# Performance work log

Measured on AMD Instinct MI355X. Metric: run time of the kernel, lower is better.

Reference implementation:

```python
import jax, jax.numpy as jnp
import numpy as np

EMBED_DIM = 1024
NUM_HEADS = 16
HEAD_DIM = EMBED_DIM // NUM_HEADS
SCALE = 1.0 / np.sqrt(HEAD_DIM)


def _quant_linear(x, w, b):
    # Per-tensor symmetric int8 quantize -> dequantize -> GEMM (faithful to QuantizedLinear)
    s = jnp.max(jnp.abs(w)) / 127.0
    w_dq = jnp.clip(jnp.round(w / s), -128.0, 127.0) * s
    return jnp.einsum('bse,oe->bso', x, w_dq) + b


def setup_inputs() -> dict:
    key = jax.random.key(0)
    ks = jax.random.split(key, 7)
    B, S, E = 2, 2048, EMBED_DIM
    return {
        'query': jax.random.normal(ks[0], (B, S, E), dtype=jnp.float32),
        'key': jax.random.normal(ks[1], (B, S, E), dtype=jnp.float32),
        'value': jax.random.normal(ks[2], (B, S, E), dtype=jnp.float32),
        'Wq': jax.random.normal(ks[3], (E, E), dtype=jnp.float32) * 0.02,
        'bq': jnp.zeros((E,), dtype=jnp.float32),
        'Wk': jax.random.normal(ks[4], (E, E), dtype=jnp.float32) * 0.02,
        'bk': jnp.zeros((E,), dtype=jnp.float32),
        'Wv': jax.random.normal(ks[5], (E, E), dtype=jnp.float32) * 0.02,
        'bv': jnp.zeros((E,), dtype=jnp.float32),
        'Wo': jax.random.normal(ks[6], (E, E), dtype=jnp.float32) * 0.02,
        'bo': jnp.zeros((E,), dtype=jnp.float32),
    }


def reference(query, key, value, Wq, bq, Wk, bk, Wv, bv, Wo, bo):
    B, S, E = query.shape
    H, D = NUM_HEADS, HEAD_DIM
    Q = _quant_linear(query, Wq, bq).reshape(B, S, H, D).transpose(0, 2, 1, 3)
    K = _quant_linear(key, Wk, bk).reshape(B, S, H, D).transpose(0, 2, 1, 3)
    V = _quant_linear(value, Wv, bv).reshape(B, S, H, D).transpose(0, 2, 1, 3)
    # [B,H,S,S] unfused attention scores
    scores = jnp.einsum('bhqd,bhkd->bhqk', Q, K) * SCALE
    attn = jax.nn.softmax(scores, axis=-1)  # dropout is identity at inference
    out = jnp.einsum('bhqk,bhkd->bhqd', attn, V)
    out = out.transpose(0, 2, 1, 3).reshape(B, S, E)
    return _quant_linear(out, Wo, bo)
```

## Files before the change

kernel.cpp:

```cpp
#include <hip/hip_runtime.h>
#include <math.h>

#define S_LEN 2048
#define EMB   1024
#define NHEAD 16
#define HDIM  64
#define MTOT  4096
#define EXP2_SCALE 0.18033688011112042f

typedef __attribute__((ext_vector_type(8))) short bf16x8;
typedef __attribute__((ext_vector_type(8))) _Float16 f16x8;
typedef __attribute__((ext_vector_type(4))) float f32x4;

#if __has_builtin(__builtin_amdgcn_exp2f)
#define FEXP2(x) __builtin_amdgcn_exp2f(x)
#else
#define FEXP2(x) exp2f(x)
#endif

__device__ __forceinline__ short f2bf(float f) {
  union { float f; unsigned u; } v; v.f = f;
  unsigned r = v.u + 0x7fffu + ((v.u >> 16) & 1u);
  return (short)(r >> 16);
}
__device__ __forceinline__ float bf2f(short s) {
  union { float f; unsigned u; } v; v.u = ((unsigned)(unsigned short)s) << 16;
  return v.f;
}
__device__ __forceinline__ short f2h(float f) {
  union { _Float16 h; short s; } u; u.h = (_Float16)f; return u.s;
}
__device__ __forceinline__ unsigned pkbf(float e0, float e1) {
  unsigned a = __float_as_uint(e1) + 0x8000u;
  unsigned b = __float_as_uint(e0) + 0x8000u;
  return __builtin_amdgcn_perm(a, b, 0x07060302u);
}

__device__ __forceinline__ void gload_lds16(const void* g, void* l) {
  __builtin_amdgcn_global_load_lds(
      (const __attribute__((address_space(1))) void*)g,
      (__attribute__((address_space(3))) void*)l, 16, 0, 0);
}

__global__ void wabsmax_k(const float* __restrict__ W0, const float* __restrict__ W1,
                          const float* __restrict__ W2, const float* __restrict__ W3,
                          unsigned* __restrict__ scaleU) {
  int w = blockIdx.x & 3;
  int part = blockIdx.x >> 2;
  const float* W = (w == 0) ? W0 : (w == 1) ? W1 : (w == 2) ? W2 : W3;
  float m = 0.f;
  int base = part * 16384;
#pragma unroll
  for (int p = 0; p < 16; ++p) {
    const float4 v = *(const float4*)&W[base + p * 1024 + threadIdx.x * 4];
    m = fmaxf(m, fmaxf(fmaxf(fabsf(v.x), fabsf(v.y)), fmaxf(fabsf(v.z), fabsf(v.w))));
  }
  __shared__ float red[256];
  red[threadIdx.x] = m;
  __syncthreads();
  for (int s = 128; s > 0; s >>= 1) {
    if (threadIdx.x < s) red[threadIdx.x] = fmaxf(red[threadIdx.x], red[threadIdx.x + s]);
    __syncthreads();
  }
  if (threadIdx.x == 0) atomicMax(&scaleU[w], __float_as_uint(red[0]));
}

__global__ void wquant_k(const float* __restrict__ W0, const float* __restrict__ W1,
                         const float* __restrict__ W2, const float* __restrict__ W3,
                         short* __restrict__ Q0, short* __restrict__ Q1,
                         short* __restrict__ Q2, short* __restrict__ Q3,
                         const unsigned* __restrict__ scaleU, float* __restrict__ sVal) {
  int w = blockIdx.y;
  const float* W = (w == 0) ? W0 : (w == 1) ? W1 : (w == 2) ? W2 : W3;
  short* Q = (w == 0) ? Q0 : (w == 1) ? Q1 : (w == 2) ? Q2 : Q3;
  float s = __uint_as_float(scaleU[w]) * (1.0f / 127.0f);
  if (blockIdx.x == 0 && threadIdx.x == 0) sVal[w] = s;
  int idx = (blockIdx.x * 256 + threadIdx.x) * 4;
  float4 v = *(const float4*)&W[idx];
  float qx = fminf(fmaxf(rintf(v.x / s), -128.f), 127.f);
  float qy = fminf(fmaxf(rintf(v.y / s), -128.f), 127.f);
  float qz = fminf(fmaxf(rintf(v.z / s), -128.f), 127.f);
  float qw = fminf(fmaxf(rintf(v.w / s), -128.f), 127.f);
  short4 q;
  if (w == 3) { q.x = f2h(qx); q.y = f2h(qy); q.z = f2h(qz); q.w = f2h(qw); }
  else        { q.x = f2bf(qx); q.y = f2bf(qy); q.z = f2bf(qz); q.w = f2bf(qw); }
  *(short4*)&Q[idx] = q;
}

__global__ void acast_k(const float* __restrict__ A0, const float* __restrict__ A1,
                        const float* __restrict__ A2,
                        short* __restrict__ H0, short* __restrict__ H1,
                        short* __restrict__ H2) {
  int w = blockIdx.y;
  const float* A = (w == 0) ? A0 : (w == 1) ? A1 : A2;
  short* H = (w == 0) ? H0 : (w == 1) ? H1 : H2;
  int idx = (blockIdx.x * 256 + threadIdx.x) * 4;
  float4 v = *(const float4*)&A[idx];
  short4 h;
  h.x = f2bf(v.x); h.y = f2bf(v.y); h.z = f2bf(v.z); h.w = f2bf(v.w);
  *(short4*)&H[idx] = h;
}

__device__ __forceinline__ void gemm_core(
    const short* __restrict__ Ah, const short* __restrict__ Bq, int m0, int n0,
    short* AhS, short* BsS, f32x4 acc[4][4]) {
  const int tid = threadIdx.x;
  const int lane = tid & 63, wave = tid >> 6;
  const int quad = lane >> 4, l16 = lane & 15;
  const int wm = wave >> 1, wn = wave & 1;

  const int swrow = lane >> 2, swcol = (lane & 3) * 8;
  const short* agh = Ah + (m0 + wave * 32 + swrow) * 1024 + swcol;
  const short* bgp = Bq + (n0 + wave * 32 + swrow) * 1024 + swcol;
  short* sA0 = AhS + wave * 1024;
  short* sB0 = BsS + wave * 1024;

  for (int k0 = 0; k0 < 1024; k0 += 32) {
    __syncthreads();
    gload_lds16(agh + k0,             sA0);
    gload_lds16(agh + 16 * 1024 + k0, sA0 + 512);
    gload_lds16(bgp + k0,             sB0);
    gload_lds16(bgp + 16 * 1024 + k0, sB0 + 512);
    __syncthreads();
    bf16x8 ah[4], bb[4];
#pragma unroll
    for (int mi = 0; mi < 4; ++mi) {
      int row = wm * 64 + mi * 16 + l16;
      ah[mi] = *(const bf16x8*)&AhS[row * 32 + quad * 8];
    }
#pragma unroll
    for (int ni = 0; ni < 4; ++ni) {
      int row = wn * 64 + ni * 16 + l16;
      bb[ni] = *(const bf16x8*)&BsS[row * 32 + quad * 8];
    }
#pragma unroll
    for (int mi = 0; mi < 4; ++mi)
#pragma unroll
      for (int ni = 0; ni < 4; ++ni)
        acc[mi][ni] = __builtin_amdgcn_mfma_f32_16x16x32_bf16(ah[mi], bb[ni], acc[mi][ni], 0, 0, 0);
  }
}

__global__ __launch_bounds__(256, 3) void gemm_qkv(
    const short* __restrict__ QA, const short* __restrict__ KA, const short* __restrict__ VA,
    const short* __restrict__ WqQ, const short* __restrict__ WkQ, const short* __restrict__ WvQ,
    const float* __restrict__ sVal,
    const float* __restrict__ bq, const float* __restrict__ bk, const float* __restrict__ bv,
    short* __restrict__ Qh, short* __restrict__ Kh, short* __restrict__ Vh) {
  __shared__ __align__(16) short AhS[128 * 32];
  __shared__ __align__(16) short BsS[128 * 32];
  const int z = blockIdx.z;
  const short* Ah = (z == 0) ? QA : (z == 1) ? KA : VA;
  const short* Bq = (z == 0) ? WqQ : (z == 1) ? WkQ : WvQ;
  const float* bias = (z == 0) ? bq : (z == 1) ? bk : bv;
  short* oh = (z == 0) ? Qh : (z == 1) ? Kh : Vh;

  const int lin = blockIdx.y * 8 + blockIdx.x;
  const int map = (lin & 7) * 32 + (lin >> 3);
  const int m0 = (map >> 3) * 128, n0 = (map & 7) * 128;
  f32x4 acc[4][4];
#pragma unroll
  for (int i = 0; i < 4; ++i)
#pragma unroll
    for (int j = 0; j < 4; ++j) acc[i][j] = (f32x4){0.f, 0.f, 0.f, 0.f};

  gemm_core(Ah, Bq, m0, n0, AhS, BsS, acc);

  const int lane = threadIdx.x & 63, wave = threadIdx.x >> 6;
  const int quad = lane >> 4, l16 = lane & 15;
  const int wm = wave >> 1, wn = wave & 1;
  float s = sVal[z];
  float post = (z == 0) ? EXP2_SCALE : 1.0f;
#pragma unroll
  for (int mi = 0; mi < 4; ++mi) {
#pragma unroll
    for (int ni = 0; ni < 4; ++ni) {
      int rowb = m0 + wm * 64 + mi * 16 + quad * 4;
      int col = n0 + wn * 64 + ni * 16 + l16;
      float bia = bias[col];
      int h = col >> 6, d = col & 63;
      if (z < 2) {
#pragma unroll
        for (int r = 0; r < 4; ++r) {
          float v = (acc[mi][ni][r] * s + bia) * post;
          int row = rowb + r;
          int b = row >> 11, sq = row & 2047;
          oh[((b * 16 + h) * 2048 + sq) * 64 + d] = f2bf(v);
        }
      } else {
        int b = rowb >> 11, sq = rowb & 2047;
        short4 pk;
        pk.x = f2bf(acc[mi][ni][0] * s + bia);
        pk.y = f2bf(acc[mi][ni][1] * s + bia);
        pk.z = f2bf(acc[mi][ni][2] * s + bia);
        pk.w = f2bf(acc[mi][ni][3] * s + bia);
        *(short4*)&oh[((b * 16 + h) * 64 + d) * 2048 + sq] = pk;
      }
    }
  }
}

__global__ __launch_bounds__(256, 2) void gemm_o(
    const short* __restrict__ OA, const short* __restrict__ WoQ,
    const float* __restrict__ sPtr, const float* __restrict__ bias,
    float* __restrict__ outF) {
  __shared__ __align__(16) short AhS[128 * 32];
  __shared__ __align__(16) short BsS[64 * 32];
  const int tid = threadIdx.x;
  const int lane = tid & 63, wave = tid >> 6;
  const int quad = lane >> 4, l16 = lane & 15;
  const int lin = blockIdx.y * 16 + blockIdx.x;
  const int map = (lin & 7) * 64 + (lin >> 3);
  const int m0 = (map >> 4) * 128, n0 = (map & 15) * 64;

  f32x4 acc[2][4];
#pragma unroll
  for (int i = 0; i < 2; ++i)
#pragma unroll
    for (int j = 0; j < 4; ++j) acc[i][j] = (f32x4){0.f, 0.f, 0.f, 0.f};

  const int swrow = lane >> 2, swcol = (lane & 3) * 8;
  const short* agh = OA + (m0 + wave * 32 + swrow) * 1024 + swcol;
  const short* bgp = WoQ + (n0 + wave * 16 + swrow) * 1024 + swcol;
  short* sA0 = AhS + wave * 1024;
  short* sB0 = BsS + wave * 512;

  for (int k0 = 0; k0 < 1024; k0 += 32) {
    __syncthreads();
    gload_lds16(agh + k0,             sA0);
    gload_lds16(agh + 16 * 1024 + k0, sA0 + 512);
    gload_lds16(bgp + k0,             sB0);
    __syncthreads();
    f16x8 ah[2], bb[4];
#pragma unroll
    for (int mi = 0; mi < 2; ++mi) {
      int row = wave * 32 + mi * 16 + l16;
      ah[mi] = *(const f16x8*)&AhS[row * 32 + quad * 8];
    }
#pragma unroll
    for (int ni = 0; ni < 4; ++ni) {
      int row = ni * 16 + l16;
      bb[ni] = *(const f16x8*)&BsS[row * 32 + quad * 8];
    }
#pragma unroll
    for (int mi = 0; mi < 2; ++mi)
#pragma unroll
      for (int ni = 0; ni < 4; ++ni)
        acc[mi][ni] = __builtin_amdgcn_mfma_f32_16x16x32_f16(ah[mi], bb[ni], acc[mi][ni], 0, 0, 0);
  }

  const float s = *sPtr;
#pragma unroll
  for (int mi = 0; mi < 2; ++mi) {
#pragma unroll
    for (int ni = 0; ni < 4; ++ni) {
      int rowb = m0 + wave * 32 + mi * 16 + quad * 4;
      int col = n0 + ni * 16 + l16;
      float bia = bias[col];
#pragma unroll
      for (int r = 0; r < 4; ++r)
        outF[(rowb + r) * 1024 + col] = acc[mi][ni][r] * s + bia;
    }
  }
}

__global__ __launch_bounds__(256, 2) void flash_k(
    const short* __restrict__ Qh, const short* __restrict__ Kh,
    const short* __restrict__ Vh,
    short* __restrict__ Oh) {
  __shared__ __align__(16) short Khs[64 * 72];
  __shared__ __align__(16) short Vhs[64 * 72];

  const int tid = threadIdx.x;
  const int lane = tid & 63, wave = tid >> 6;
  const int quad = lane >> 4, l16 = lane & 15;
  const int bh = blockIdx.y;
  const int b = bh >> 4, h = bh & 15;
  const int q0 = blockIdx.x * 128 + wave * 32;
  const int qkbase = bh * (S_LEN * HDIM);
  const int vbase  = bh * (HDIM * S_LEN);

  bf16x8 qb[2][2];
#pragma unroll
  for (int g = 0; g < 2; ++g) {
    const int qrow = qkbase + (q0 + g * 16 + l16) * HDIM;
    qb[g][0] = *(const bf16x8*)&Qh[qrow + quad * 8];
    qb[g][1] = *(const bf16x8*)&Qh[qrow + 32 + quad * 8];
  }

  f32x4 zero = {0.f, 0.f, 0.f, 0.f};
  f32x4 oacc[2][4];
#pragma unroll
  for (int g = 0; g < 2; ++g)
#pragma unroll
    for (int i = 0; i < 4; ++i) oacc[g][i] = zero;
  f32x4 sacc[2] = {zero, zero};

  union { bf16x8 v; unsigned u[4]; } ones_;
  ones_.u[0] = ones_.u[1] = ones_.u[2] = ones_.u[3] = 0x3F803F80u;

  const int sr  = wave * 16 + l16;
  const int sc8 = quad * 8;
  const int srP = (sr & 32) | (((sr >> 2) & 1) << 4) | (((sr >> 3) & 3) << 2) | (sr & 3);
  const int kgl = qkbase + sr * HDIM + sc8;
  const int vgl = vbase + sr * S_LEN + sc8;
  const int kOff = srP * 72 + sc8;
  const int vOff = sr * 72 + sc8;

  bf16x8 pk0 = *(const bf16x8*)&Kh[kgl];
  bf16x8 pk1 = *(const bf16x8*)&Kh[kgl + 32];
  bf16x8 pv0 = *(const bf16x8*)&Vh[vgl];
  bf16x8 pv1 = *(const bf16x8*)&Vh[vgl + 32];

  for (int kt = 0; kt < S_LEN; kt += 64) {
    __syncthreads();
    *(bf16x8*)&Khs[kOff]      = pk0;
    *(bf16x8*)&Khs[kOff + 32] = pk1;
    *(bf16x8*)&Vhs[vOff]      = pv0;
    *(bf16x8*)&Vhs[vOff + 32] = pv1;
    __syncthreads();
    if (kt + 64 < S_LEN) {
      int kg = kgl + (kt + 64) * HDIM;
      int vg = vgl + (kt + 64);
      pk0 = *(const bf16x8*)&Kh[kg];
      pk1 = *(const bf16x8*)&Kh[kg + 32];
      pv0 = *(const bf16x8*)&Vh[vg];
      pv1 = *(const bf16x8*)&Vh[vg + 32];
    }
    f32x4 sc[2][4];
#pragma unroll
    for (int nj = 0; nj < 4; ++nj) {
      const int kr = nj * 16 + l16;
      bf16x8 kf0 = *(const bf16x8*)&Khs[kr * 72 + quad * 8];
      bf16x8 kf1 = *(const bf16x8*)&Khs[kr * 72 + 32 + quad * 8];
#pragma unroll
      for (int g = 0; g < 2; ++g) {
        f32x4 sv = zero;
        sv = __builtin_amdgcn_mfma_f32_16x16x32_bf16(kf0, qb[g][0], sv, 0, 0, 0);
        sv = __builtin_amdgcn_mfma_f32_16x16x32_bf16(kf1, qb[g][1], sv, 0, 0, 0);
        sc[g][nj] = sv;
      }
    }
#pragma unroll
    for (int g = 0; g < 2; ++g)
#pragma unroll
      for (int nj = 0; nj < 4; ++nj)
#pragma unroll
        for (int r = 0; r < 4; ++r)
          sc[g][nj][r] = FEXP2(sc[g][nj][r]);
    union { bf16x8 v; unsigned u[4]; } P[2][2];
#pragma unroll
    for (int g = 0; g < 2; ++g) {
      P[g][0].u[0] = pkbf(sc[g][0][0], sc[g][0][1]);
      P[g][0].u[1] = pkbf(sc[g][0][2], sc[g][0][3]);
      P[g][0].u[2] = pkbf(sc[g][1][0], sc[g][1][1]);
      P[g][0].u[3] = pkbf(sc[g][1][2], sc[g][1][3]);
      P[g][1].u[0] = pkbf(sc[g][2][0], sc[g][2][1]);
      P[g][1].u[1] = pkbf(sc[g][2][2], sc[g][2][3]);
      P[g][1].u[2] = pkbf(sc[g][3][0], sc[g][3][1]);
      P[g][1].u[3] = pkbf(sc[g][3][2], sc[g][3][3]);
    }
#pragma unroll
    for (int g = 0; g < 2; ++g) {
      sacc[g] = __builtin_amdgcn_mfma_f32_16x16x32_bf16(P[g][0].v, ones_.v, sacc[g], 0, 0, 0);
      sacc[g] = __builtin_amdgcn_mfma_f32_16x16x32_bf16(P[g][1].v, ones_.v, sacc[g], 0, 0, 0);
    }
#pragma unroll
    for (int ni = 0; ni < 4; ++ni) {
      int vr = ni * 16 + l16;
      bf16x8 vf0 = *(const bf16x8*)&Vhs[vr * 72 + quad * 8];
      bf16x8 vf1 = *(const bf16x8*)&Vhs[vr * 72 + 32 + quad * 8];
#pragma unroll
      for (int g = 0; g < 2; ++g) {
        oacc[g][ni] = __builtin_amdgcn_mfma_f32_16x16x32_bf16(P[g][0].v, vf0, oacc[g][ni], 0, 0, 0);
        oacc[g][ni] = __builtin_amdgcn_mfma_f32_16x16x32_bf16(P[g][1].v, vf1, oacc[g][ni], 0, 0, 0);
      }
    }
  }
#pragma unroll
  for (int g = 0; g < 2; ++g) {
#pragma unroll
    for (int r = 0; r < 4; ++r) {
      float inv = 1.f / sacc[g][r];
      int row = b * S_LEN + q0 + g * 16 + quad * 4 + r;
#pragma unroll
      for (int ni = 0; ni < 4; ++ni) {
        float v = oacc[g][ni][r] * inv;
        int idx = row * 1024 + h * 64 + ni * 16 + l16;
        Oh[idx] = f2h(v);
      }
    }
  }
}

extern "C" void kernel_launch(void* const* d_in, const int* in_sizes, int n_in,
                              void* d_out, int out_size, void* d_ws, size_t ws_size,
                              hipStream_t stream) {
  const float* query = (const float*)d_in[0];
  const float* key_i = (const float*)d_in[1];
  const float* value = (const float*)d_in[2];
  const float* Wq = (const float*)d_in[3];
  const float* bq = (const float*)d_in[4];
  const float* Wk = (const float*)d_in[5];
  const float* bk = (const float*)d_in[6];
  const float* Wv = (const float*)d_in[7];
  const float* bv = (const float*)d_in[8];
  const float* Wo = (const float*)d_in[9];
  const float* bo = (const float*)d_in[10];
  float* out = (float*)d_out;

  char* w = (char*)d_ws;
  unsigned* scaleU = (unsigned*)w;
  float* sVal = (float*)(w + 256);
  size_t off = 512;
  const size_t SZ_W = 2097152;
  const size_t SZ_A = 8388608;
  short* WqQ = (short*)(w + off); off += SZ_W;
  short* WkQ = (short*)(w + off); off += SZ_W;
  short* WvQ = (short*)(w + off); off += SZ_W;
  short* WoQ = (short*)(w + off); off += SZ_W;
  short* Qa  = (short*)(w + off); off += SZ_A;
  short* Ka  = (short*)(w + off); off += SZ_A;
  short* Va  = (short*)(w + off); off += SZ_A;
  short* Qh  = (short*)(w + off); off += SZ_A;
  short* Kh  = (short*)(w + off); off += SZ_A;
  short* Vh  = (short*)(w + off); off += SZ_A;
  short* Oh  = Qa;

  (void)hipMemsetAsync(scaleU, 0, 16, stream);
  wabsmax_k<<<256, 256, 0, stream>>>(Wq, Wk, Wv, Wo, scaleU);
  wquant_k<<<dim3(1024, 4), 256, 0, stream>>>(Wq, Wk, Wv, Wo, WqQ, WkQ, WvQ, WoQ, scaleU, sVal);
  acast_k<<<dim3(4096, 3), 256, 0, stream>>>(query, key_i, value, Qa, Ka, Va);
  gemm_qkv<<<dim3(8, 32, 3), 256, 0, stream>>>(Qa, Ka, Va, WqQ, WkQ, WvQ, sVal,
                                               bq, bk, bv, Qh, Kh, Vh);
  flash_k<<<dim3(16, 32), 256, 0, stream>>>(Qh, Kh, Vh, Oh);
  gemm_o<<<dim3(16, 32), 256, 0, stream>>>(Oh, WoQ, sVal + 3, bo, out);
}
```

Baseline: 222.8 us.

## Merge weight quant and activation cast kernels; double GEMM K-step to 64

```diff
diff --git a/kernel.cpp b/kernel.cpp
--- a/kernel.cpp
+++ b/kernel.cpp
@@ -65,40 +65,42 @@
   if (threadIdx.x == 0) atomicMax(&scaleU[w], __float_as_uint(red[0]));
 }
 
-__global__ void wquant_k(const float* __restrict__ W0, const float* __restrict__ W1,
-                         const float* __restrict__ W2, const float* __restrict__ W3,
-                         short* __restrict__ Q0, short* __restrict__ Q1,
-                         short* __restrict__ Q2, short* __restrict__ Q3,
-                         const unsigned* __restrict__ scaleU, float* __restrict__ sVal) {
-  int w = blockIdx.y;
-  const float* W = (w == 0) ? W0 : (w == 1) ? W1 : (w == 2) ? W2 : W3;
-  short* Q = (w == 0) ? Q0 : (w == 1) ? Q1 : (w == 2) ? Q2 : Q3;
-  float s = __uint_as_float(scaleU[w]) * (1.0f / 127.0f);
-  if (blockIdx.x == 0 && threadIdx.x == 0) sVal[w] = s;
-  int idx = (blockIdx.x * 256 + threadIdx.x) * 4;
-  float4 v = *(const float4*)&W[idx];
-  float qx = fminf(fmaxf(rintf(v.x / s), -128.f), 127.f);
-  float qy = fminf(fmaxf(rintf(v.y / s), -128.f), 127.f);
-  float qz = fminf(fmaxf(rintf(v.z / s), -128.f), 127.f);
-  float qw = fminf(fmaxf(rintf(v.w / s), -128.f), 127.f);
-  short4 q;
-  if (w == 3) { q.x = f2h(qx); q.y = f2h(qy); q.z = f2h(qz); q.w = f2h(qw); }
-  else        { q.x = f2bf(qx); q.y = f2bf(qy); q.z = f2bf(qz); q.w = f2bf(qw); }
-  *(short4*)&Q[idx] = q;
-}
-
-__global__ void acast_k(const float* __restrict__ A0, const float* __restrict__ A1,
-                        const float* __restrict__ A2,
-                        short* __restrict__ H0, short* __restrict__ H1,
-                        short* __restrict__ H2) {
-  int w = blockIdx.y;
-  const float* A = (w == 0) ? A0 : (w == 1) ? A1 : A2;
-  short* H = (w == 0) ? H0 : (w == 1) ? H1 : H2;
-  int idx = (blockIdx.x * 256 + threadIdx.x) * 4;
-  float4 v = *(const float4*)&A[idx];
-  short4 h;
-  h.x = f2bf(v.x); h.y = f2bf(v.y); h.z = f2bf(v.z); h.w = f2bf(v.w);
-  *(short4*)&H[idx] = h;
+__global__ void wqa_k(const float* __restrict__ W0, const float* __restrict__ W1,
+                      const float* __restrict__ W2, const float* __restrict__ W3,
+                      short* __restrict__ Q0, short* __restrict__ Q1,
+                      short* __restrict__ Q2, short* __restrict__ Q3,
+                      const float* __restrict__ A0, const float* __restrict__ A1,
+                      const float* __restrict__ A2,
+                      short* __restrict__ H0, short* __restrict__ H1,
+                      short* __restrict__ H2,
+                      const unsigned* __restrict__ scaleU, float* __restrict__ sVal) {
+  int y = blockIdx.y;
+  if (y < 4) {
+    if (blockIdx.x >= 1024) return;
+    const float* W = (y == 0) ? W0 : (y == 1) ? W1 : (y == 2) ? W2 : W3;
+    short* Q = (y == 0) ? Q0 : (y == 1) ? Q1 : (y == 2) ? Q2 : Q3;
+    float s = __uint_as_float(scaleU[y]) * (1.0f / 127.0f);
+    if (blockIdx.x == 0 && threadIdx.x == 0) sVal[y] = s;
+    int idx = (blockIdx.x * 256 + threadIdx.x) * 4;
+    float4 v = *(const float4*)&W[idx];
+    float qx = fminf(fmaxf(rintf(v.x / s), -128.f), 127.f);
+    float qy = fminf(fmaxf(rintf(v.y / s), -128.f), 127.f);
+    float qz = fminf(fmaxf(rintf(v.z / s), -128.f), 127.f);
+    float qw = fminf(fmaxf(rintf(v.w / s), -128.f), 127.f);
+    short4 q;
+    if (y == 3) { q.x = f2h(qx); q.y = f2h(qy); q.z = f2h(qz); q.w = f2h(qw); }
+    else        { q.x = f2bf(qx); q.y = f2bf(qy); q.z = f2bf(qz); q.w = f2bf(qw); }
+    *(short4*)&Q[idx] = q;
+  } else {
+    int w = y - 4;
+    const float* A = (w == 0) ? A0 : (w == 1) ? A1 : A2;
+    short* H = (w == 0) ? H0 : (w == 1) ? H1 : H2;
+    int idx = (blockIdx.x * 256 + threadIdx.x) * 4;
+    float4 v = *(const float4*)&A[idx];
+    short4 h;
+    h.x = f2bf(v.x); h.y = f2bf(v.y); h.z = f2bf(v.z); h.w = f2bf(v.w);
+    *(short4*)&H[idx] = h;
+  }
 }
 
 __device__ __forceinline__ void gemm_core(
@@ -115,40 +117,48 @@
   short* sA0 = AhS + wave * 1024;
   short* sB0 = BsS + wave * 1024;
 
-  for (int k0 = 0; k0 < 1024; k0 += 32) {
-    __syncthreads();
-    gload_lds16(agh + k0,             sA0);
-    gload_lds16(agh + 16 * 1024 + k0, sA0 + 512);
-    gload_lds16(bgp + k0,             sB0);
-    gload_lds16(bgp + 16 * 1024 + k0, sB0 + 512);
-    __syncthreads();
-    bf16x8 ah[4], bb[4];
+  for (int k0 = 0; k0 < 1024; k0 += 64) {
+    __syncthreads();
+    gload_lds16(agh + k0,                  sA0);
+    gload_lds16(agh + 16 * 1024 + k0,      sA0 + 512);
+    gload_lds16(agh + k0 + 32,             sA0 + 4096);
+    gload_lds16(agh + 16 * 1024 + k0 + 32, sA0 + 4096 + 512);
+    gload_lds16(bgp + k0,                  sB0);
+    gload_lds16(bgp + 16 * 1024 + k0,      sB0 + 512);
+    gload_lds16(bgp + k0 + 32,             sB0 + 4096);
+    gload_lds16(bgp + 16 * 1024 + k0 + 32, sB0 + 4096 + 512);
+    __syncthreads();
+    bf16x8 ah[4][2], bb[4][2];
 #pragma unroll
     for (int mi = 0; mi < 4; ++mi) {
       int row = wm * 64 + mi * 16 + l16;
-      ah[mi] = *(const bf16x8*)&AhS[row * 32 + quad * 8];
+      ah[mi][0] = *(const bf16x8*)&AhS[row * 32 + quad * 8];
+      ah[mi][1] = *(const bf16x8*)&AhS[4096 + row * 32 + quad * 8];
     }
 #pragma unroll
     for (int ni = 0; ni < 4; ++ni) {
       int row = wn * 64 + ni * 16 + l16;
-      bb[ni] = *(const bf16x8*)&BsS[row * 32 + quad * 8];
+      bb[ni][0] = *(const bf16x8*)&BsS[row * 32 + quad * 8];
+      bb[ni][1] = *(const bf16x8*)&BsS[4096 + row * 32 + quad * 8];
     }
 #pragma unroll
     for (int mi = 0; mi < 4; ++mi)
 #pragma unroll
-      for (int ni = 0; ni < 4; ++ni)
-        acc[mi][ni] = __builtin_amdgcn_mfma_f32_16x16x32_bf16(ah[mi], bb[ni], acc[mi][ni], 0, 0, 0);
-  }
-}
-
-__global__ __launch_bounds__(256, 3) void gemm_qkv(
+      for (int ni = 0; ni < 4; ++ni) {
+        acc[mi][ni] = __builtin_amdgcn_mfma_f32_16x16x32_bf16(ah[mi][0], bb[ni][0], acc[mi][ni], 0, 0, 0);
+        acc[mi][ni] = __builtin_amdgcn_mfma_f32_16x16x32_bf16(ah[mi][1], bb[ni][1], acc[mi][ni], 0, 0, 0);
+      }
+  }
+}
+
+__global__ __launch_bounds__(256, 2) void gemm_qkv(
     const short* __restrict__ QA, const short* __restrict__ KA, const short* __restrict__ VA,
     const short* __restrict__ WqQ, const short* __restrict__ WkQ, const short* __restrict__ WvQ,
     const float* __restrict__ sVal,
     const float* __restrict__ bq, const float* __restrict__ bk, const float* __restrict__ bv,
     short* __restrict__ Qh, short* __restrict__ Kh, short* __restrict__ Vh) {
-  __shared__ __align__(16) short AhS[128 * 32];
-  __shared__ __align__(16) short BsS[128 * 32];
+  __shared__ __align__(16) short AhS[2 * 128 * 32];
+  __shared__ __align__(16) short BsS[2 * 128 * 32];
   const int z = blockIdx.z;
   const short* Ah = (z == 0) ? QA : (z == 1) ? KA : VA;
   const short* Bq = (z == 0) ? WqQ : (z == 1) ? WkQ : WvQ;
@@ -204,8 +214,8 @@
     const short* __restrict__ OA, const short* __restrict__ WoQ,
     const float* __restrict__ sPtr, const float* __restrict__ bias,
     float* __restrict__ outF) {
-  __shared__ __align__(16) short AhS[128 * 32];
-  __shared__ __align__(16) short BsS[64 * 32];
+  __shared__ __align__(16) short AhS[2 * 128 * 32];
+  __shared__ __align__(16) short BsS[2 * 64 * 32];
   const int tid = threadIdx.x;
   const int lane = tid & 63, wave = tid >> 6;
   const int quad = lane >> 4, l16 = lane & 15;
@@ -225,28 +235,35 @@
   short* sA0 = AhS + wave * 1024;
   short* sB0 = BsS + wave * 512;
 
-  for (int k0 = 0; k0 < 1024; k0 += 32) {
-    __syncthreads();
-    gload_lds16(agh + k0,             sA0);
-    gload_lds16(agh + 16 * 1024 + k0, sA0 + 512);
-    gload_lds16(bgp + k0,             sB0);
-    __syncthreads();
-    f16x8 ah[2], bb[4];
+  for (int k0 = 0; k0 < 1024; k0 += 64) {
+    __syncthreads();
+    gload_lds16(agh + k0,                  sA0);
+    gload_lds16(agh + 16 * 1024 + k0,      sA0 + 512);
+    gload_lds16(agh + k0 + 32,             sA0 + 4096);
+    gload_lds16(agh + 16 * 1024 + k0 + 32, sA0 + 4096 + 512);
+    gload_lds16(bgp + k0,                  sB0);
+    gload_lds16(bgp + k0 + 32,             sB0 + 2048);
+    __syncthreads();
+    f16x8 ah[2][2], bb[4][2];
 #pragma unroll
     for (int mi = 0; mi < 2; ++mi) {
       int row = wave * 32 + mi * 16 + l16;
-      ah[mi] = *(const f16x8*)&AhS[row * 32 + quad * 8];
+      ah[mi][0] = *(const f16x8*)&AhS[row * 32 + quad * 8];
+      ah[mi][1] = *(const f16x8*)&AhS[4096 + row * 32 + quad * 8];
     }
 #pragma unroll
     for (int ni = 0; ni < 4; ++ni) {
       int row = ni * 16 + l16;
-      bb[ni] = *(const f16x8*)&BsS[row * 32 + quad * 8];
+      bb[ni][0] = *(const f16x8*)&BsS[row * 32 + quad * 8];
+      bb[ni][1] = *(const f16x8*)&BsS[2048 + row * 32 + quad * 8];
     }
 #pragma unroll
     for (int mi = 0; mi < 2; ++mi)
 #pragma unroll
-      for (int ni = 0; ni < 4; ++ni)
-        acc[mi][ni] = __builtin_amdgcn_mfma_f32_16x16x32_f16(ah[mi], bb[ni], acc[mi][ni], 0, 0, 0);
+      for (int ni = 0; ni < 4; ++ni) {
+        acc[mi][ni] = __builtin_amdgcn_mfma_f32_16x16x32_f16(ah[mi][0], bb[ni][0], acc[mi][ni], 0, 0, 0);
+        acc[mi][ni] = __builtin_amdgcn_mfma_f32_16x16x32_f16(ah[mi][1], bb[ni][1], acc[mi][ni], 0, 0, 0);
+      }
   }
 
   const float s = *sPtr;
@@ -429,8 +446,9 @@
 
   (void)hipMemsetAsync(scaleU, 0, 16, stream);
   wabsmax_k<<<256, 256, 0, stream>>>(Wq, Wk, Wv, Wo, scaleU);
-  wquant_k<<<dim3(1024, 4), 256, 0, stream>>>(Wq, Wk, Wv, Wo, WqQ, WkQ, WvQ, WoQ, scaleU, sVal);
-  acast_k<<<dim3(4096, 3), 256, 0, stream>>>(query, key_i, value, Qa, Ka, Va);
+  wqa_k<<<dim3(4096, 7), 256, 0, stream>>>(Wq, Wk, Wv, Wo, WqQ, WkQ, WvQ, WoQ,
+                                           query, key_i, value, Qa, Ka, Va,
+                                           scaleU, sVal);
   gemm_qkv<<<dim3(8, 32, 3), 256, 0, stream>>>(Qa, Ka, Va, WqQ, WkQ, WvQ, sVal,
                                                bq, bk, bv, Qh, Kh, Vh);
   flash_k<<<dim3(16, 32), 256, 0, stream>>>(Qh, Kh, Vh, Oh);
```

New measurement: 219.4 us. No clear change (-1.5%).
